# Performance work log

Measured on AMD Instinct MI355X. Metric: run time of the kernel, lower is better.

The kernel has to match this reference:

```python
import jax, jax.numpy as jnp
import numpy as np

NUM_HEADS = 8
HEAD_DIM = 16


def setup_inputs() -> dict:
    key = jax.random.key(0)
    ks = jax.random.split(key, 9)
    B, S, E, H = 2, 4096, 16, 128
    sc_in = 1.0 / np.sqrt(E)
    sc_h = 1.0 / np.sqrt(H)
    return {
        "x": jax.random.normal(ks[0], (B, S, E), dtype=jnp.float32),
        "wq": jax.random.normal(ks[1], (H, E), dtype=jnp.float32) * sc_in,
        "bq": jax.random.normal(ks[2], (H,), dtype=jnp.float32) * 0.02,
        "wk": jax.random.normal(ks[3], (H, E), dtype=jnp.float32) * sc_in,
        "bk": jax.random.normal(ks[4], (H,), dtype=jnp.float32) * 0.02,
        "wv": jax.random.normal(ks[5], (H, E), dtype=jnp.float32) * sc_in,
        "bv": jax.random.normal(ks[6], (H,), dtype=jnp.float32) * 0.02,
        "wo": jax.random.normal(ks[7], (E, H), dtype=jnp.float32) * sc_h,
        "bo": jax.random.normal(ks[8], (E,), dtype=jnp.float32) * 0.02,
    }


def reference(x, wq, bq, wk, bk, wv, bv, wo, bo):
    B, S, E = x.shape
    H = wq.shape[0]
    nh, hd = NUM_HEADS, HEAD_DIM
    # QKV projections (torch Linear: y = x @ W.T + b)
    q = x @ wq.T + bq  # [B,S,H]
    k = x @ wk.T + bk
    v = x @ wv.T + bv
    # split heads -> [B,nh,S,hd]
    q = q.reshape(B, S, nh, hd).transpose(0, 2, 1, 3)
    k = k.reshape(B, S, nh, hd).transpose(0, 2, 1, 3)
    v = v.reshape(B, S, nh, hd).transpose(0, 2, 1, 3)
    # flex_attention with block_mask=None == full SDPA, scale = 1/sqrt(head_dim)
    scale = 1.0 / np.sqrt(hd)
    scores = jnp.einsum("bhqd,bhkd->bhqk", q, k) * scale  # [B,nh,S,S]
    attn = jax.nn.softmax(scores, axis=-1)
    out = jnp.einsum("bhqk,bhkd->bhqd", attn, v)  # [B,nh,S,hd]
    out = out.transpose(0, 2, 1, 3).reshape(B, S, H)
    return out @ wo.T + bo
```

## Files before the change

### kernel.cpp

```cpp
#include <hip/hip_runtime.h>
#include <hip/hip_bf16.h>
#include <math.h>

#define NH 8
#define HD 16
#define EE 16
#define HH 128
#define NCH 4
#define QR 16

typedef __attribute__((ext_vector_type(8)))  short short8;
typedef __attribute__((ext_vector_type(16))) float f32x16;
typedef __attribute__((ext_vector_type(4)))  float f32x4;

#define EXP2F(x) __builtin_amdgcn_exp2f(x)

__global__ __launch_bounds__(256) void qkv_fused(
        const float* __restrict__ x,
        const float* __restrict__ wq, const float* __restrict__ bq,
        const float* __restrict__ wk, const float* __restrict__ bk,
        const float* __restrict__ wv, const float* __restrict__ bv,
        __hip_bfloat16* __restrict__ Qb, __hip_bfloat16* __restrict__ Kb,
        __hip_bfloat16* __restrict__ Vt, float* __restrict__ OutZero, int S) {
    int row0 = blockIdx.x * QR;
    int b = row0 / S, s0 = row0 - b * S;
    int tid = threadIdx.x;

    OutZero[(size_t)blockIdx.x * 256 + tid] = 0.f;

    __shared__ __align__(16) float xs[QR][EE];
    __shared__ __align__(16) short qsb[QR][136];
    __shared__ __align__(16) short ksb[QR][136];
    __shared__ __align__(16) short vsb[QR][136];

    ((float*)xs)[tid] = x[(size_t)row0 * EE + tid];
    __syncthreads();

    int h = tid & 127, sub = tid >> 7;
    float wqr[16], wkr[16], wvr[16];
    const float4* wq4 = (const float4*)(wq + h * EE);
    const float4* wk4 = (const float4*)(wk + h * EE);
    const float4* wv4 = (const float4*)(wv + h * EE);
#pragma unroll
    for (int j = 0; j < 4; ++j) {
        float4 a = wq4[j]; wqr[4*j]=a.x; wqr[4*j+1]=a.y; wqr[4*j+2]=a.z; wqr[4*j+3]=a.w;
        float4 c = wk4[j]; wkr[4*j]=c.x; wkr[4*j+1]=c.y; wkr[4*j+2]=c.z; wkr[4*j+3]=c.w;
        float4 d = wv4[j]; wvr[4*j]=d.x; wvr[4*j+1]=d.y; wvr[4*j+2]=d.z; wvr[4*j+3]=d.w;
    }
    float bqv = bq[h], bkv = bk[h], bvv = bv[h];

#pragma unroll
    for (int rr = 0; rr < 8; ++rr) {
        int r = (sub << 3) + rr;
        const float4* xv = (const float4*)xs[r];
        float aq = bqv, ak = bkv, av = bvv;
#pragma unroll
        for (int j = 0; j < 4; ++j) {
            float4 xe = xv[j];
            aq += xe.x*wqr[4*j] + xe.y*wqr[4*j+1] + xe.z*wqr[4*j+2] + xe.w*wqr[4*j+3];
            ak += xe.x*wkr[4*j] + xe.y*wkr[4*j+1] + xe.z*wkr[4*j+2] + xe.w*wkr[4*j+3];
            av += xe.x*wvr[4*j] + xe.y*wvr[4*j+1] + xe.z*wvr[4*j+2] + xe.w*wvr[4*j+3];
        }
        __hip_bfloat16 qb = __float2bfloat16(aq * 0.36067376022f);
        __hip_bfloat16 kb = __float2bfloat16(ak);
        __hip_bfloat16 vb = __float2bfloat16(av);
        qsb[r][h] = *reinterpret_cast<short*>(&qb);
        ksb[r][h] = *reinterpret_cast<short*>(&kb);
        vsb[r][h] = *reinterpret_cast<short*>(&vb);
    }
    __syncthreads();

    {
        int pr = tid & 127;
        int r = pr & 15, head = pr >> 4;
        if (tid < 128) {
            short8 a = *(const short8*)&qsb[r][head * 16];
            short8 c = *(const short8*)&qsb[r][head * 16 + 8];
            short* dst = (short*)Qb + ((size_t)(b * NH + head) * S + s0 + r) * HD;
            *(short8*)dst = a;
            *(short8*)(dst + 8) = c;
        } else {
            short8 a = *(const short8*)&ksb[r][head * 16];
            short8 c = *(const short8*)&ksb[r][head * 16 + 8];
            short* dst = (short*)Kb + ((size_t)(b * NH + head) * S + s0 + r) * HD;
            *(short8*)dst = a;
            *(short8*)(dst + 8) = c;
        }
    }
    {
        int hd_idx = tid >> 1;
        int head2 = hd_idx >> 4, d2 = hd_idx & 15;
        int si0 = (tid & 1) * 8;
        short8 w0;
#pragma unroll
        for (int j = 0; j < 8; ++j) w0[j] = vsb[si0 + j][hd_idx];
        short* dst = (short*)Vt + ((size_t)(b * NH + head2) * HD + d2) * S + s0 + si0;
        *(short8*)dst = w0;
    }
}

__global__ __launch_bounds__(256, 8) void attn(const __hip_bfloat16* __restrict__ Qb,
                                               const __hip_bfloat16* __restrict__ Kb,
                                               const __hip_bfloat16* __restrict__ Vtb,
                                               const float* __restrict__ wo,
                                               const float* __restrict__ bo,
                                               float* __restrict__ Out,
                                               int S, int BH) {
    int blk = blockIdx.x;
    int bh = blk & (16 - 1);
    int q0 = (blk >> 4) * 32;
    int cb = threadIdx.x >> 6;
    int lane = threadIdx.x & 63;
    int ql = lane & 31, half = lane >> 5;
    int l15 = lane & 15, l4 = lane >> 4;
    int CS = S / NCH;
    int kbeg = cb * CS;

    __shared__ __align__(16) union {
        short pt[NCH][32 * 40];
        struct { float o[NCH][32][16]; float l[NCH][32]; } red;
    } sm;
    __shared__ __align__(16) float onorm[32][16];
    short* pt = sm.pt[cb];

    const short* qptr = (const short*)Qb + ((size_t)bh * S + q0) * HD;
    const short* kf_ptr = (const short*)Kb + ((size_t)bh * S + kbeg + ql) * HD + 8 * half;
    const short* vf_ptr = (const short*)Vtb + ((size_t)bh * HD + l15) * S + kbeg + 8 * l4;

    short8 qf = *(const short8*)(qptr + ql * HD + 8 * half);

    f32x16 zc;
#pragma unroll
    for (int i = 0; i < 16; ++i) zc[i] = 0.f;

    float l = 0.f;
    f32x4 o0, o1;
#pragma unroll
    for (int i = 0; i < 4; ++i) { o0[i] = 0.f; o1[i] = 0.f; }

    int wswz = ((ql >> 3) & 3) << 3;
    int rswz0 = ((l15 >> 3) & 3) << 3;
    int rswz1 = (((l15 + 16) >> 3) & 3) << 3;

    for (int it = 0; it < CS / 32; ++it) {
        short8 kf = *(const short8*)kf_ptr;
        kf_ptr += 32 * HD;
        f32x16 st = __builtin_amdgcn_mfma_f32_32x32x16_bf16(kf, qf, zc, 0, 0, 0);

        float pf[16];
#pragma unroll
        for (int r = 0; r < 16; ++r) pf[r] = EXP2F(st[r]);
        float rs = ((pf[0] + pf[1]) + (pf[2] + pf[3])) + ((pf[4] + pf[5]) + (pf[6] + pf[7]))
                 + ((pf[8] + pf[9]) + (pf[10] + pf[11])) + ((pf[12] + pf[13]) + (pf[14] + pf[15]));
        l += rs;

        union PU { __hip_bfloat162 b2; unsigned u; };
        unsigned pk[8];
#pragma unroll
        for (int i = 0; i < 8; ++i) {
            float2 f2; f2.x = pf[2 * i]; f2.y = pf[2 * i + 1];
            PU pu; pu.b2 = __float22bfloat162_rn(f2);
            pk[i] = pu.u;
        }
#pragma unroll
        for (int i = 0; i < 4; ++i) {
            uint2 w; w.x = pk[2 * i]; w.y = pk[2 * i + 1];
            *(uint2*)&pt[ql * 40 + ((8 * i + 4 * half) ^ wswz)] = w;
        }
        short8 p0 = *(const short8*)&pt[l15 * 40 + ((8 * l4) ^ rswz0)];
        short8 p1 = *(const short8*)&pt[(l15 + 16) * 40 + ((8 * l4) ^ rswz1)];
        short8 vf = *(const short8*)vf_ptr;
        vf_ptr += 32;

        o0 = __builtin_amdgcn_mfma_f32_16x16x32_bf16(vf, p0, o0, 0, 0, 0);
        o1 = __builtin_amdgcn_mfma_f32_16x16x32_bf16(vf, p1, o1, 0, 0, 0);
    }

    l += __shfl_xor(l, 32);

    __syncthreads();
    {
        float4 r0; r0.x = o0[0]; r0.y = o0[1]; r0.z = o0[2]; r0.w = o0[3];
        float4 r1; r1.x = o1[0]; r1.y = o1[1]; r1.z = o1[2]; r1.w = o1[3];
        *(float4*)&sm.red.o[cb][l15][4 * l4]      = r0;
        *(float4*)&sm.red.o[cb][l15 + 16][4 * l4] = r1;
        if (half == 0) sm.red.l[cb][ql] = l;
    }
    __syncthreads();

    if (threadIdx.x < 128) {
        int q = threadIdx.x >> 2, quad = threadIdx.x & 3;
        float4 acc; acc.x = 0.f; acc.y = 0.f; acc.z = 0.f; acc.w = 0.f;
        float ls = 0.f;
#pragma unroll
        for (int c = 0; c < NCH; ++c) {
            float4 v = *(const float4*)&sm.red.o[c][q][4 * quad];
            acc.x += v.x; acc.y += v.y; acc.z += v.z; acc.w += v.w;
            ls += sm.red.l[c][q];
        }
        float inv = 1.f / ls;
        acc.x *= inv; acc.y *= inv; acc.z *= inv; acc.w *= inv;
        *(float4*)&onorm[q][4 * quad] = acc;
    }
    __syncthreads();

    int b = bh >> 3, head = bh & 7;
#pragma unroll
    for (int i = 0; i < 2; ++i) {
        int p = threadIdx.x + 256 * i;
        int q = p >> 4, e = p & 15;
        const float4* w4 = (const float4*)(wo + e * HH + head * HD);
        const float4* o4 = (const float4*)&onorm[q][0];
        float acc = bo[e] * (1.0f / NH);
#pragma unroll
        for (int j = 0; j < 4; ++j) {
            float4 w = w4[j];
            float4 o = o4[j];
            acc += w.x * o.x + w.y * o.y + w.z * o.z + w.w * o.w;
        }
        atomicAdd(&Out[((size_t)(b * S + q0 + q)) * EE + e], acc);
    }
}

extern "C" void kernel_launch(void* const* d_in, const int* in_sizes, int n_in,
                              void* d_out, int out_size, void* d_ws, size_t ws_size,
                              hipStream_t stream) {
    const float* x  = (const float*)d_in[0];
    const float* wq = (const float*)d_in[1];
    const float* bq = (const float*)d_in[2];
    const float* wk = (const float*)d_in[3];
    const float* bk = (const float*)d_in[4];
    const float* wv = (const float*)d_in[5];
    const float* bv = (const float*)d_in[6];
    const float* wo = (const float*)d_in[7];
    const float* bo = (const float*)d_in[8];
    float* out = (float*)d_out;

    int rows = in_sizes[0] / EE;
    int S = 4096;
    int B = rows / S;
    int BH = B * NH;

    size_t n = (size_t)rows * HH;
    __hip_bfloat16* Qb = (__hip_bfloat16*)d_ws;
    __hip_bfloat16* Kb = Qb + n;
    __hip_bfloat16* Vt = Kb + n;

    qkv_fused<<<rows / QR, 256, 0, stream>>>(x, wq, bq, wk, bk, wv, bv, Qb, Kb, Vt, out, S);
    attn<<<(S / 32) * BH, 256, 0, stream>>>(Qb, Kb, Vt, wo, bo, out, S, BH);
}
```

Before: 122.8 us.

## Keep P in registers via lane shuffles and fold row-sum into PV MFMA

Replaces the LDS round-trip that transposed the bf16 probability tile with cross-half lane shuffles, so P feeds the PV matmul directly from registers. The PV product switches from two 16x16x32 MFMAs to two 32x32x16 MFMAs whose extra rows (lanes 16-31) load a constant vector of bf16 ones, so the softmax denominator falls out of the MFMA and the scalar row-sum adds go away. This removes LDS stores and loads and the 16-add reduction per iteration. The cost is shuffle traffic, larger MFMAs that are half wasted, a row sum taken from bf16-rounded P, and removal of the occupancy hint in launch_bounds.

Result: slower. 140.9 us (+14.7%).

```diff
diff --git a/kernel.cpp b/kernel.cpp
--- a/kernel.cpp
+++ b/kernel.cpp
@@ -99,92 +99,97 @@
     }
 }
 
-__global__ __launch_bounds__(256, 8) void attn(const __hip_bfloat16* __restrict__ Qb,
-                                               const __hip_bfloat16* __restrict__ Kb,
-                                               const __hip_bfloat16* __restrict__ Vtb,
-                                               const float* __restrict__ wo,
-                                               const float* __restrict__ bo,
-                                               float* __restrict__ Out,
-                                               int S, int BH) {
+__global__ __launch_bounds__(256) void attn(const __hip_bfloat16* __restrict__ Qb,
+                                            const __hip_bfloat16* __restrict__ Kb,
+                                            const __hip_bfloat16* __restrict__ Vtb,
+                                            const float* __restrict__ wo,
+                                            const float* __restrict__ bo,
+                                            float* __restrict__ Out,
+                                            int S, int BH) {
     int blk = blockIdx.x;
     int bh = blk & (16 - 1);
     int q0 = (blk >> 4) * 32;
     int cb = threadIdx.x >> 6;
     int lane = threadIdx.x & 63;
     int ql = lane & 31, half = lane >> 5;
-    int l15 = lane & 15, l4 = lane >> 4;
     int CS = S / NCH;
     int kbeg = cb * CS;
 
-    __shared__ __align__(16) union {
-        short pt[NCH][32 * 40];
-        struct { float o[NCH][32][16]; float l[NCH][32]; } red;
-    } sm;
+    __shared__ __align__(16) struct {
+        float o[NCH][32][16];
+        float l[NCH][32];
+    } red;
     __shared__ __align__(16) float onorm[32][16];
-    short* pt = sm.pt[cb];
 
     const short* qptr = (const short*)Qb + ((size_t)bh * S + q0) * HD;
     const short* kf_ptr = (const short*)Kb + ((size_t)bh * S + kbeg + ql) * HD + 8 * half;
-    const short* vf_ptr = (const short*)Vtb + ((size_t)bh * HD + l15) * S + kbeg + 8 * l4;
+    const short* vf_ptr = (const short*)Vtb + ((size_t)bh * HD + (ql & 15)) * S + kbeg + 8 * half;
+    bool vload = (ql < 16);
 
     short8 qf = *(const short8*)(qptr + ql * HD + 8 * half);
 
+    short8 ones8;
+#pragma unroll
+    for (int j = 0; j < 8; ++j) ones8[j] = (short)0x3F80;
+
     f32x16 zc;
 #pragma unroll
     for (int i = 0; i < 16; ++i) zc[i] = 0.f;
 
-    float l = 0.f;
-    f32x4 o0, o1;
-#pragma unroll
-    for (int i = 0; i < 4; ++i) { o0[i] = 0.f; o1[i] = 0.f; }
-
-    int wswz = ((ql >> 3) & 3) << 3;
-    int rswz0 = ((l15 >> 3) & 3) << 3;
-    int rswz1 = (((l15 + 16) >> 3) & 3) << 3;
+    f32x16 o;
+#pragma unroll
+    for (int i = 0; i < 16; ++i) o[i] = 0.f;
 
     for (int it = 0; it < CS / 32; ++it) {
         short8 kf = *(const short8*)kf_ptr;
         kf_ptr += 32 * HD;
+        short8 vf0 = ones8, vf1 = ones8;
+        if (vload) {
+            vf0 = *(const short8*)vf_ptr;
+            vf1 = *(const short8*)(vf_ptr + 16);
+        }
+        vf_ptr += 32;
+
         f32x16 st = __builtin_amdgcn_mfma_f32_32x32x16_bf16(kf, qf, zc, 0, 0, 0);
 
         float pf[16];
 #pragma unroll
         for (int r = 0; r < 16; ++r) pf[r] = EXP2F(st[r]);
-        float rs = ((pf[0] + pf[1]) + (pf[2] + pf[3])) + ((pf[4] + pf[5]) + (pf[6] + pf[7]))
-                 + ((pf[8] + pf[9]) + (pf[10] + pf[11])) + ((pf[12] + pf[13]) + (pf[14] + pf[15]));
-        l += rs;
 
         union PU { __hip_bfloat162 b2; unsigned u; };
-        unsigned pk[8];
+        int pk[8];
 #pragma unroll
         for (int i = 0; i < 8; ++i) {
             float2 f2; f2.x = pf[2 * i]; f2.y = pf[2 * i + 1];
             PU pu; pu.b2 = __float22bfloat162_rn(f2);
-            pk[i] = pu.u;
-        }
-#pragma unroll
-        for (int i = 0; i < 4; ++i) {
-            uint2 w; w.x = pk[2 * i]; w.y = pk[2 * i + 1];
-            *(uint2*)&pt[ql * 40 + ((8 * i + 4 * half) ^ wswz)] = w;
-        }
-        short8 p0 = *(const short8*)&pt[l15 * 40 + ((8 * l4) ^ rswz0)];
-        short8 p1 = *(const short8*)&pt[(l15 + 16) * 40 + ((8 * l4) ^ rswz1)];
-        short8 vf = *(const short8*)vf_ptr;
-        vf_ptr += 32;
-
-        o0 = __builtin_amdgcn_mfma_f32_16x16x32_bf16(vf, p0, o0, 0, 0, 0);
-        o1 = __builtin_amdgcn_mfma_f32_16x16x32_bf16(vf, p1, o1, 0, 0, 0);
-    }
-
-    l += __shfl_xor(l, 32);
-
-    __syncthreads();
+            pk[i] = (int)pu.u;
+        }
+        int xpk[8];
+#pragma unroll
+        for (int i = 0; i < 8; ++i) xpk[i] = __shfl_xor(pk[i], 32);
+
+        uint4 b0, b1;
+        b0.x = half ? xpk[2] : pk[0];
+        b0.y = half ? xpk[3] : pk[1];
+        b0.z = half ? pk[2]  : xpk[0];
+        b0.w = half ? pk[3]  : xpk[1];
+        b1.x = half ? xpk[6] : pk[4];
+        b1.y = half ? xpk[7] : pk[5];
+        b1.z = half ? pk[6]  : xpk[4];
+        b1.w = half ? pk[7]  : xpk[5];
+        short8 p0 = *(short8*)&b0;
+        short8 p1 = *(short8*)&b1;
+
+        o = __builtin_amdgcn_mfma_f32_32x32x16_bf16(vf0, p0, o, 0, 0, 0);
+        o = __builtin_amdgcn_mfma_f32_32x32x16_bf16(vf1, p1, o, 0, 0, 0);
+    }
+
     {
-        float4 r0; r0.x = o0[0]; r0.y = o0[1]; r0.z = o0[2]; r0.w = o0[3];
-        float4 r1; r1.x = o1[0]; r1.y = o1[1]; r1.z = o1[2]; r1.w = o1[3];
-        *(float4*)&sm.red.o[cb][l15][4 * l4]      = r0;
-        *(float4*)&sm.red.o[cb][l15 + 16][4 * l4] = r1;
-        if (half == 0) sm.red.l[cb][ql] = l;
+        float4 d0; d0.x = o[0]; d0.y = o[1]; d0.z = o[2]; d0.w = o[3];
+        float4 d1; d1.x = o[4]; d1.y = o[5]; d1.z = o[6]; d1.w = o[7];
+        *(float4*)&red.o[cb][ql][4 * half]     = d0;
+        *(float4*)&red.o[cb][ql][8 + 4 * half] = d1;
+        if (half == 0) red.l[cb][ql] = o[8];
     }
     __syncthreads();
 
@@ -194,9 +199,9 @@
         float ls = 0.f;
 #pragma unroll
         for (int c = 0; c < NCH; ++c) {
-            float4 v = *(const float4*)&sm.red.o[c][q][4 * quad];
+            float4 v = *(const float4*)&red.o[c][q][4 * quad];
             acc.x += v.x; acc.y += v.y; acc.z += v.z; acc.w += v.w;
-            ls += sm.red.l[c][q];
+            ls += red.l[c][q];
         }
         float inv = 1.f / ls;
         acc.x *= inv; acc.y *= inv; acc.z *= inv; acc.w *= inv;
@@ -215,8 +220,8 @@
 #pragma unroll
         for (int j = 0; j < 4; ++j) {
             float4 w = w4[j];
-            float4 o = o4[j];
-            acc += w.x * o.x + w.y * o.y + w.z * o.z + w.w * o.w;
+            float4 ov = o4[j];
+            acc += w.x * ov.x + w.y * ov.y + w.z * ov.z + w.w * ov.w;
         }
         atomicAdd(&Out[((size_t)(b * S + q0 + q)) * EE + e], acc);
     }
```
